# Kernel tuning notes

Measured on AMD Instinct MI355X. Metric: run time of the kernel, lower is better.

The kernel has to match this reference:

```python
import jax, jax.numpy as jnp
import numpy as np

N_NODES = 50000
N_EDGES = 800000
D_NODE = 64
D_EDGE = 64
D_OUT = 64
D_HID = 128
LN_EPS = 1e-5


def _mlp_params(key, d_in):
    # layer sizes: [d_in, D_HID, D_HID, D_OUT]; weights stored [in, out]
    ks = jax.random.split(key, 3)
    dims = [d_in, D_HID, D_HID, D_OUT]
    params = []
    for i in range(3):
        s = 1.0 / np.sqrt(dims[i])
        params.append(jax.random.uniform(ks[i], (dims[i], dims[i + 1]), minval=-s, maxval=s, dtype=jnp.float32))
        params.append(jnp.zeros((dims[i + 1],), jnp.float32))
    # LayerNorm gamma/beta
    params.append(jnp.ones((D_OUT,), jnp.float32))
    params.append(jnp.zeros((D_OUT,), jnp.float32))
    return params


def _mlp_ln(h, W0, b0, W1, b1, W2, b2, g, beta):
    h = jax.nn.relu(h @ W0 + b0)
    h = jax.nn.relu(h @ W1 + b1)
    h = h @ W2 + b2
    mu = jnp.mean(h, axis=-1, keepdims=True)
    var = jnp.mean(jnp.square(h - mu), axis=-1, keepdims=True)
    return (h - mu) * jax.lax.rsqrt(var + LN_EPS) * g + beta


def setup_inputs() -> dict:
    key = jax.random.key(0)
    k = jax.random.split(key, 8)
    inp = {
        "x": jax.random.normal(k[0], (N_NODES, D_NODE), jnp.float32),
        "mesh_edge_index": jax.random.randint(k[1], (2, N_EDGES), 0, N_NODES, dtype=jnp.int32),
        "mesh_edge_attr": jax.random.normal(k[2], (N_EDGES, D_EDGE), jnp.float32),
        "world_edge_index": jax.random.randint(k[3], (2, N_EDGES), 0, N_NODES, dtype=jnp.int32),
        "world_edge_attr": jax.random.normal(k[4], (N_EDGES, D_EDGE), jnp.float32),
    }
    names = ["W0", "b0", "W1", "b1", "W2", "b2", "ln_g", "ln_b"]
    for pref, kk, d_in in [("mesh", k[5], 2 * D_NODE + D_EDGE),
                           ("world", k[6], 2 * D_NODE + D_EDGE),
                           ("upd", k[7], D_NODE + 2 * D_OUT)]:
        ps = _mlp_params(kk, d_in)
        for nm, p in zip(names, ps):
            inp[f"{pref}_{nm}"] = p
    return inp


def _edge_block(x, edge_index, edge_attr, W0, b0, W1, b1, W2, b2, g, beta):
    src, dst = edge_index[0], edge_index[1]  # PyG: x_j = source, x_i = target
    x_i = x[dst]  # [E, D_NODE]
    x_j = x[src]
    concat = jnp.concatenate([x_i, x_j, edge_attr], axis=-1)  # [E, 2D+De]
    new_edge = edge_attr + _mlp_ln(concat, W0, b0, W1, b1, W2, b2, g, beta)
    agg = jax.ops.segment_sum(new_edge, dst, num_segments=N_NODES)  # 'add' aggr at target
    return agg, new_edge


def reference(x, mesh_edge_index, mesh_edge_attr, world_edge_index, world_edge_attr,
              mesh_W0, mesh_b0, mesh_W1, mesh_b1, mesh_W2, mesh_b2, mesh_ln_g, mesh_ln_b,
              world_W0, world_b0, world_W1, world_b1, world_W2, world_b2, world_ln_g, world_ln_b,
              upd_W0, upd_b0, upd_W1, upd_b1, upd_W2, upd_b2, upd_ln_g, upd_ln_b):
    agg_m, new_edge_m = _edge_block(x, mesh_edge_index, mesh_edge_attr,
                                    mesh_W0, mesh_b0, mesh_W1, mesh_b1, mesh_W2, mesh_b2, mesh_ln_g, mesh_ln_b)
    agg_w, new_edge_w = _edge_block(x, world_edge_index, world_edge_attr,
                                    world_W0, world_b0, world_W1, world_b1, world_W2, world_b2, world_ln_g, world_ln_b)
    concat = jnp.concatenate([x, agg_m, agg_w], axis=-1)  # [N, D_NODE + 2*D_OUT]
    x_new = x + _mlp_ln(concat, upd_W0, upd_b0, upd_W1, upd_b1, upd_W2, upd_b2, upd_ln_g, upd_ln_b)
    return x_new, new_edge_m, new_edge_w
```

## Files before the change

kernel.cpp:

```cpp
#include <hip/hip_runtime.h>


#define NNODES 50000
#define NEDGES 800000
#define NBLK 512

typedef __bf16 bf16x8 __attribute__((ext_vector_type(8)));
typedef float f32x4 __attribute__((ext_vector_type(4)));
#define MFMA(a, b, c) __builtin_amdgcn_mfma_f32_16x16x32_bf16(a, b, c, 0, 0, 0)

#define OFF_A 0
#define OFF_H0 24576
#define OFF_O OFF_H0
#define OFF_SA 40960
#define OFF_P 57600
#define OFF_IX 59648
#define OFF_PAR 59904
#define SMEM 61696

__device__ __forceinline__ unsigned short f2bf(float f) {
  unsigned u = __builtin_bit_cast(unsigned, f);
  u = (u + 0x7fffu + ((u >> 16) & 1u)) >> 16;
  return (unsigned short)u;
}
__device__ __forceinline__ float bf2f(unsigned short h) {
  return __builtin_bit_cast(float, (unsigned)h << 16);
}
__device__ __forceinline__ unsigned long long pk4(f32x4 v) {
  union { unsigned short h[4]; unsigned long long u; } p;
  p.h[0] = f2bf(v[0]); p.h[1] = f2bf(v[1]); p.h[2] = f2bf(v[2]); p.h[3] = f2bf(v[3]);
  return p.u;
}
__device__ __forceinline__ void cvt8s(float4 f0, float4 f1, char* d) {
  union { unsigned short us[8]; int4 v; } u;
  u.us[0] = f2bf(f0.x); u.us[1] = f2bf(f0.y); u.us[2] = f2bf(f0.z); u.us[3] = f2bf(f0.w);
  u.us[4] = f2bf(f1.x); u.us[5] = f2bf(f1.y); u.us[6] = f2bf(f1.z); u.us[7] = f2bf(f1.w);
  *(int4*)d = u.v;
}

template <bool EDGE>
__global__ __launch_bounds__(512, 4) void mlp_block(
    const float* __restrict__ g1, const float* __restrict__ g2,
    const float* __restrict__ g3, const int* __restrict__ srcI,
    const int* __restrict__ dstI, const unsigned short* __restrict__ Wt,
    const float* __restrict__ b0, const float* __restrict__ b1,
    const float* __restrict__ b2, const float* __restrict__ gam,
    const float* __restrict__ bet, float* __restrict__ outp,
    float* __restrict__ agg, int M) {
  __shared__ __align__(16) char sm[SMEM];
  const int tid = threadIdx.x, lane = tid & 63, wave = tid >> 6;
  const int lrow = lane & 15, cg = lane >> 4;
  const unsigned short* Wt0 = Wt;
  const unsigned short* Wt1 = Wt + 24576;
  const unsigned short* Wt2 = Wt + 40960;
  const int ntiles = (M + 63) >> 6;

  const int cg2 = wave & 3, rg = wave >> 2;

  for (int i = tid; i < 448; i += 512) {
    float v;
    if (i < 128) v = b0[i];
    else if (i < 256) v = b1[i - 128];
    else if (i < 320) v = b2[i - 256];
    else if (i < 384) v = gam[i - 320];
    else v = bet[i - 384];
    ((float*)(sm + OFF_PAR))[i] = v;
  }
  const float* PAR = (const float*)(sm + OFF_PAR);

  bf16x8 w0f[6], w1f[4], w2f[4];
#pragma unroll
  for (int kk = 0; kk < 6; ++kk)
    w0f[kk] = *(const bf16x8*)(Wt0 + (wave * 16 + lrow) * 192 + kk * 32 + cg * 8);
#pragma unroll
  for (int kk = 0; kk < 4; ++kk)
    w1f[kk] = *(const bf16x8*)(Wt1 + (wave * 16 + lrow) * 128 + kk * 32 + cg * 8);
#pragma unroll
  for (int kk = 0; kk < 4; ++kk)
    w2f[kk] = *(const bf16x8*)(Wt2 + (cg2 * 16 + lrow) * 128 + kk * 32 + cg * 8);

  const int srow = (tid >> 5) * 4 + ((tid & 31) >> 3), oct = tid & 7;

  int t = blockIdx.x;
  if (t >= ntiles) return;

  float4 ga0, ga1, gb0, gb1;
  int dcur = 0;
  {
    int row = t * 64 + srow;
    int r1, r2;
    if (EDGE) { dcur = dstI[row]; r1 = dcur; r2 = srcI[row]; }
    else { int rr = min(row, M - 1); r1 = rr; r2 = rr; }
    const float* p1 = g1 + (size_t)r1 * 64 + oct * 8;
    const float* p2 = g2 + (size_t)r2 * 64 + oct * 8;
    ga0 = *(const float4*)p1; ga1 = *(const float4*)(p1 + 4);
    gb0 = *(const float4*)p2; gb1 = *(const float4*)(p2 + 4);
#pragma unroll
    for (int i = 0; i < 2; ++i) {
      int chunk = wave * 2 + i;
      const float* gsrc;
      if (EDGE) gsrc = g3 + (size_t)t * 4096 + chunk * 256 + lane * 4;
      else { int gr = min(t * 64 + chunk * 4 + (lane >> 4), M - 1); gsrc = g3 + (size_t)gr * 64 + (lane & 15) * 4; }
      __builtin_amdgcn_global_load_lds((const __attribute__((address_space(1))) unsigned int*)gsrc,
          (__attribute__((address_space(3))) unsigned int*)(sm + OFF_SA + chunk * 1040), 16, 0, 0);
    }
  }

  for (; t < ntiles; t += NBLK) {
    const int tn = t + NBLK;
    const bool more = tn < ntiles;
    __syncthreads();
    {
      char* a0 = sm + OFF_A + srow * 384;
      const int swz = (srow & 7) << 4;
      cvt8s(ga0, ga1, a0 + ((oct * 16) ^ swz));
      cvt8s(gb0, gb1, a0 + ((128 + oct * 16) ^ swz));
      const char* sa = sm + OFF_SA + (srow >> 2) * 1040 + (srow & 3) * 256 + oct * 32;
      float4 c0 = *(const float4*)sa, c1 = *(const float4*)(sa + 16);
      cvt8s(c0, c1, a0 + ((256 + oct * 16) ^ swz));
      if (EDGE && (tid & 7) == 0) ((int*)(sm + OFF_IX))[srow] = dcur;
    }
    int dn = 0, sn = 0;
    if (EDGE && more) { int row = tn * 64 + srow; dn = dstI[row]; sn = srcI[row]; }
    __syncthreads();
    if (more) {
      const float *p1, *p2;
      if (EDGE) {
        p1 = g1 + (size_t)dn * 64 + oct * 8;
        p2 = g2 + (size_t)sn * 64 + oct * 8;
        dcur = dn;
      } else {
        int rr = min(tn * 64 + srow, M - 1);
        p1 = g1 + (size_t)rr * 64 + oct * 8;
        p2 = g2 + (size_t)rr * 64 + oct * 8;
      }
      ga0 = *(const float4*)p1; ga1 = *(const float4*)(p1 + 4);
      gb0 = *(const float4*)p2; gb1 = *(const float4*)(p2 + 4);
#pragma unroll
      for (int i = 0; i < 2; ++i) {
        int chunk = wave * 2 + i;
        const float* gsrc;
        if (EDGE) gsrc = g3 + (size_t)tn * 4096 + chunk * 256 + lane * 4;
        else { int gr = min(tn * 64 + chunk * 4 + (lane >> 4), M - 1); gsrc = g3 + (size_t)gr * 64 + (lane & 15) * 4; }
        __builtin_amdgcn_global_load_lds((const __attribute__((address_space(1))) unsigned int*)gsrc,
            (__attribute__((address_space(3))) unsigned int*)(sm + OFF_SA + chunk * 1040), 16, 0, 0);
      }
    }
    {
      const f32x4 bb0 = *(const f32x4*)(PAR + wave * 16 + cg * 4);
#pragma unroll
      for (int rt = 0; rt < 4; ++rt) {
        const int row = rt * 16 + lrow, swz = (row & 7) << 4;
        const char* ab = sm + OFF_A + row * 384;
        f32x4 acc = {0.f, 0.f, 0.f, 0.f};
#pragma unroll
        for (int kk = 0; kk < 6; ++kk)
          acc = MFMA(w0f[kk], *(const bf16x8*)(ab + ((kk * 64 + cg * 16) ^ swz)), acc);
        f32x4 h;
#pragma unroll
        for (int q = 0; q < 4; ++q) h[q] = fmaxf(acc[q] + bb0[q], 0.f);
        *(unsigned long long*)(sm + OFF_H0 + row * 256 + ((wave * 32 + cg * 8) ^ swz)) = pk4(h);
      }
    }
    __syncthreads();
    {
      const f32x4 bb1 = *(const f32x4*)(PAR + 128 + wave * 16 + cg * 4);
#pragma unroll
      for (int rt = 0; rt < 4; ++rt) {
        const int row = rt * 16 + lrow, swz = (row & 7) << 4;
        const char* hb = sm + OFF_H0 + row * 256;
        f32x4 acc = {0.f, 0.f, 0.f, 0.f};
#pragma unroll
        for (int kk = 0; kk < 4; ++kk)
          acc = MFMA(w1f[kk], *(const bf16x8*)(hb + ((kk * 64 + cg * 16) ^ swz)), acc);
        f32x4 h;
#pragma unroll
        for (int q = 0; q < 4; ++q) h[q] = fmaxf(acc[q] + bb1[q], 0.f);
        *(unsigned long long*)(sm + OFF_A + row * 384 + ((wave * 32 + cg * 8) ^ swz)) = pk4(h);
      }
    }
    __syncthreads();
    f32x4 accE[2];
    {
      const f32x4 bb2 = *(const f32x4*)(PAR + 256 + cg2 * 16 + cg * 4);
#pragma unroll
      for (int j = 0; j < 2; ++j) {
        const int rt = rg * 2 + j, row = rt * 16 + lrow, swz = (row & 7) << 4;
        const char* hb = sm + OFF_A + row * 384;
        f32x4 acc = {0.f, 0.f, 0.f, 0.f};
#pragma unroll
        for (int kk = 0; kk < 4; ++kk)
          acc = MFMA(w2f[kk], *(const bf16x8*)(hb + ((kk * 64 + cg * 16) ^ swz)), acc);
#pragma unroll
        for (int q = 0; q < 4; ++q) acc[q] += bb2[q];
        float s = acc[0] + acc[1] + acc[2] + acc[3];
        float ss = acc[0] * acc[0] + acc[1] * acc[1] + acc[2] * acc[2] + acc[3] * acc[3];
        s += __shfl_xor(s, 16, 64); s += __shfl_xor(s, 32, 64);
        ss += __shfl_xor(ss, 16, 64); ss += __shfl_xor(ss, 32, 64);
        if (cg == 0) *(float2*)(sm + OFF_P + row * 32 + cg2 * 8) = make_float2(s, ss);
        accE[j] = acc;
      }
    }
    __syncthreads();
    {
      const f32x4 gv = *(const f32x4*)(PAR + 320 + cg2 * 16 + cg * 4);
      const f32x4 bv = *(const f32x4*)(PAR + 384 + cg2 * 16 + cg * 4);
#pragma unroll
      for (int j = 0; j < 2; ++j) {
        const int rt = rg * 2 + j, row = rt * 16 + lrow;
        float4 p0 = *(const float4*)(sm + OFF_P + row * 32);
        float4 p1 = *(const float4*)(sm + OFF_P + row * 32 + 16);
        float s = p0.x + p0.z + p1.x + p1.z, ss = p0.y + p0.w + p1.y + p1.w;
        float mean = s * (1.f / 64.f);
        float var = fmaxf(ss * (1.f / 64.f) - mean * mean, 0.f);
        float inv = rsqrtf(var + 1e-5f);
        const int swz = (row & 7) << 4;
        unsigned long long rv =
            *(const unsigned long long*)(sm + OFF_A + row * 384 + ((256 + cg2 * 32 + cg * 8) ^ swz));
        f32x4 a = accE[j];
        f32x4 o;
        o[0] = (a[0] - mean) * inv * gv[0] + bv[0] + bf2f((unsigned short)rv);
        o[1] = (a[1] - mean) * inv * gv[1] + bv[1] + bf2f((unsigned short)(rv >> 16));
        o[2] = (a[2] - mean) * inv * gv[2] + bv[2] + bf2f((unsigned short)(rv >> 32));
        o[3] = (a[3] - mean) * inv * gv[3] + bv[3] + bf2f((unsigned short)(rv >> 48));
        *(f32x4*)(sm + OFF_O + row * 256 + ((cg2 * 64 + cg * 16) ^ ((row & 15) << 4))) = o;
      }
    }
    __syncthreads();
#pragma unroll
    for (int j = 0; j < 2; ++j) {
      const int row = wave * 8 + j * 4 + cg, gr = t * 64 + row;
      const int cq = lrow;
      const bool ok = EDGE || gr < M;
      f32x4 v = *(const f32x4*)(sm + OFF_O + row * 256 + ((cq * 16) ^ ((row & 15) << 4)));
      if (ok) *(f32x4*)(outp + (size_t)gr * 64 + cq * 4) = v;
      if (EDGE) {
        const int d = ((const int*)(sm + OFF_IX))[row];
        float* ap = agg + (size_t)d * 64;
#pragma unroll
        for (int k = 0; k < 4; ++k) {
          float sv = *(const float*)(sm + OFF_O + row * 256 + (((cq + k * 16) * 4) ^ ((row & 15) << 4)));
          atomicAdd(ap + cq + k * 16, sv);
        }
      }
    }
  }
}

struct PrepArgs { const float* w[9]; unsigned short* wt[3]; };

__global__ void prep_w(PrepArgs pa) {
  int i = blockIdx.x * 256 + threadIdx.x;
  if (i >= 3 * 49152) return;
  int mlp = i / 49152;
  int rem = i - mlp * 49152;
  int mat, off, K, N;
  if (rem < 24576)      { mat = 0; off = 0;     K = 192; N = 128; }
  else if (rem < 40960) { mat = 1; off = 24576; K = 128; N = 128; }
  else                  { mat = 2; off = 40960; K = 128; N = 64;  }
  int local = rem - off;
  int n = local / K, k = local - n * K;
  if (mlp == 2 && mat == 0) k = (k + 64) % 192;
  pa.wt[mlp][rem] = f2bf(pa.w[mlp * 3 + mat][k * N + n]);
}

__global__ void zero_f4(float4* p, int n) {
  int i = blockIdx.x * blockDim.x + threadIdx.x;
  if (i < n) p[i] = make_float4(0.f, 0.f, 0.f, 0.f);
}

extern "C" void kernel_launch(void* const* d_in, const int* in_sizes, int n_in,
                              void* d_out, int out_size, void* d_ws, size_t ws_size,
                              hipStream_t stream) {
  const float* x      = (const float*)d_in[0];
  const int*   meIdx  = (const int*)d_in[1];
  const float* meAttr = (const float*)d_in[2];
  const int*   weIdx  = (const int*)d_in[3];
  const float* weAttr = (const float*)d_in[4];

  float* out_x  = (float*)d_out;
  float* out_em = out_x + (size_t)NNODES * 64;
  float* out_ew = out_em + (size_t)NEDGES * 64;

  char* ws = (char*)d_ws;
  unsigned short* WtM = (unsigned short*)ws;
  unsigned short* WtW = (unsigned short*)(ws + 98304);
  unsigned short* WtU = (unsigned short*)(ws + 196608);
  float* aggm = (float*)(ws + 294912);
  float* aggw = aggm + (size_t)NNODES * 64;

  zero_f4<<<dim3(6250), dim3(256), 0, stream>>>((float4*)aggm, 1600000);

  PrepArgs pa;
  for (int m = 0; m < 3; ++m)
    for (int l = 0; l < 3; ++l)
      pa.w[m * 3 + l] = (const float*)d_in[5 + m * 8 + l * 2];
  pa.wt[0] = WtM; pa.wt[1] = WtW; pa.wt[2] = WtU;
  prep_w<<<dim3(576), dim3(256), 0, stream>>>(pa);

  mlp_block<true><<<dim3(NBLK), dim3(512), 0, stream>>>(
      x, x, meAttr, meIdx, meIdx + NEDGES, WtM,
      (const float*)d_in[6], (const float*)d_in[8], (const float*)d_in[10],
      (const float*)d_in[11], (const float*)d_in[12],
      out_em, aggm, NEDGES);
  mlp_block<true><<<dim3(NBLK), dim3(512), 0, stream>>>(
      x, x, weAttr, weIdx, weIdx + NEDGES, WtW,
      (const float*)d_in[14], (const float*)d_in[16], (const float*)d_in[18],
      (const float*)d_in[19], (const float*)d_in[20],
      out_ew, aggw, NEDGES);
  mlp_block<false><<<dim3(NBLK), dim3(512), 0, stream>>>(
      aggm, aggw, x, nullptr, nullptr, WtU,
      (const float*)d_in[22], (const float*)d_in[24], (const float*)d_in[26],
      (const float*)d_in[27], (const float*)d_in[28],
      out_x, nullptr, NNODES);
}
```

Before: 890.2 us.

## Counting-sort edges by destination and pre-reduce segments before atomic scatter

Adds histogram, scan and scatter kernels that build a destination-sorted permutation of edges for each edge set. The edge MLP kernels then read edges through this permutation and write outputs back to their original positions. Consecutive rows with the same destination inside a tile are summed in shared memory, so only one atomicAdd per run is issued instead of one per edge. This is meant to cut the global atomic traffic of the segment sum. In exchange it adds three preprocessing kernels, including a weakly parallel two-block scan, and turns the edge-attribute loads and output stores into indirect accesses.

```diff
diff --git a/kernel.cpp b/kernel.cpp
--- a/kernel.cpp
+++ b/kernel.cpp
@@ -42,7 +42,8 @@
 __global__ __launch_bounds__(512, 4) void mlp_block(
     const float* __restrict__ g1, const float* __restrict__ g2,
     const float* __restrict__ g3, const int* __restrict__ srcI,
-    const int* __restrict__ dstI, const unsigned short* __restrict__ Wt,
+    const int* __restrict__ perm, const int* __restrict__ dstS,
+    const unsigned short* __restrict__ Wt,
     const float* __restrict__ b0, const float* __restrict__ b1,
     const float* __restrict__ b2, const float* __restrict__ gam,
     const float* __restrict__ bet, float* __restrict__ outp,
@@ -89,8 +90,11 @@
   {
     int row = t * 64 + srow;
     int r1, r2;
-    if (EDGE) { dcur = dstI[row]; r1 = dcur; r2 = srcI[row]; }
-    else { int rr = min(row, M - 1); r1 = rr; r2 = rr; }
+    if (EDGE) {
+      int e = perm[row];
+      dcur = dstS[row];
+      r1 = dcur; r2 = srcI[e];
+    } else { int rr = min(row, M - 1); r1 = rr; r2 = rr; }
     const float* p1 = g1 + (size_t)r1 * 64 + oct * 8;
     const float* p2 = g2 + (size_t)r2 * 64 + oct * 8;
     ga0 = *(const float4*)p1; ga1 = *(const float4*)(p1 + 4);
@@ -99,8 +103,10 @@
     for (int i = 0; i < 2; ++i) {
       int chunk = wave * 2 + i;
       const float* gsrc;
-      if (EDGE) gsrc = g3 + (size_t)t * 4096 + chunk * 256 + lane * 4;
-      else { int gr = min(t * 64 + chunk * 4 + (lane >> 4), M - 1); gsrc = g3 + (size_t)gr * 64 + (lane & 15) * 4; }
+      if (EDGE) {
+        int er = perm[t * 64 + chunk * 4 + (lane >> 4)];
+        gsrc = g3 + (size_t)er * 64 + (lane & 15) * 4;
+      } else { int gr = min(t * 64 + chunk * 4 + (lane >> 4), M - 1); gsrc = g3 + (size_t)gr * 64 + (lane & 15) * 4; }
       __builtin_amdgcn_global_load_lds((const __attribute__((address_space(1))) unsigned int*)gsrc,
           (__attribute__((address_space(3))) unsigned int*)(sm + OFF_SA + chunk * 1040), 16, 0, 0);
     }
@@ -121,7 +127,11 @@
       if (EDGE && (tid & 7) == 0) ((int*)(sm + OFF_IX))[srow] = dcur;
     }
     int dn = 0, sn = 0;
-    if (EDGE && more) { int row = tn * 64 + srow; dn = dstI[row]; sn = srcI[row]; }
+    if (EDGE && more) {
+      int row = tn * 64 + srow;
+      int e = perm[row];
+      dn = dstS[row]; sn = srcI[e];
+    }
     __syncthreads();
     if (more) {
       const float *p1, *p2;
@@ -140,8 +150,10 @@
       for (int i = 0; i < 2; ++i) {
         int chunk = wave * 2 + i;
         const float* gsrc;
-        if (EDGE) gsrc = g3 + (size_t)tn * 4096 + chunk * 256 + lane * 4;
-        else { int gr = min(tn * 64 + chunk * 4 + (lane >> 4), M - 1); gsrc = g3 + (size_t)gr * 64 + (lane & 15) * 4; }
+        if (EDGE) {
+          int er = perm[tn * 64 + chunk * 4 + (lane >> 4)];
+          gsrc = g3 + (size_t)er * 64 + (lane & 15) * 4;
+        } else { int gr = min(tn * 64 + chunk * 4 + (lane >> 4), M - 1); gsrc = g3 + (size_t)gr * 64 + (lane & 15) * 4; }
         __builtin_amdgcn_global_load_lds((const __attribute__((address_space(1))) unsigned int*)gsrc,
             (__attribute__((address_space(3))) unsigned int*)(sm + OFF_SA + chunk * 1040), 16, 0, 0);
       }
@@ -231,17 +243,39 @@
     for (int j = 0; j < 2; ++j) {
       const int row = wave * 8 + j * 4 + cg, gr = t * 64 + row;
       const int cq = lrow;
-      const bool ok = EDGE || gr < M;
       f32x4 v = *(const f32x4*)(sm + OFF_O + row * 256 + ((cq * 16) ^ ((row & 15) << 4)));
-      if (ok) *(f32x4*)(outp + (size_t)gr * 64 + cq * 4) = v;
       if (EDGE) {
-        const int d = ((const int*)(sm + OFF_IX))[row];
-        float* ap = agg + (size_t)d * 64;
-#pragma unroll
-        for (int k = 0; k < 4; ++k) {
-          float sv = *(const float*)(sm + OFF_O + row * 256 + (((cq + k * 16) * 4) ^ ((row & 15) << 4)));
-          atomicAdd(ap + cq + k * 16, sv);
+        const int e = perm[gr];
+        *(f32x4*)(outp + (size_t)e * 64 + cq * 4) = v;
+        const int* ix = (const int*)(sm + OFF_IX);
+        const int d = ix[row];
+        const bool head = (row == 0) || (ix[row - 1] != d);
+        if (head) {
+          float a0, a1, a2, a3;
+          {
+            const int swz = (row & 15) << 4;
+            a0 = *(const float*)(sm + OFF_O + row * 256 + ((cq * 4) ^ swz));
+            a1 = *(const float*)(sm + OFF_O + row * 256 + (((cq + 16) * 4) ^ swz));
+            a2 = *(const float*)(sm + OFF_O + row * 256 + (((cq + 32) * 4) ^ swz));
+            a3 = *(const float*)(sm + OFF_O + row * 256 + (((cq + 48) * 4) ^ swz));
+          }
+          int r2 = row + 1;
+          while (r2 < 64 && ix[r2] == d) {
+            const int swz = (r2 & 15) << 4;
+            a0 += *(const float*)(sm + OFF_O + r2 * 256 + ((cq * 4) ^ swz));
+            a1 += *(const float*)(sm + OFF_O + r2 * 256 + (((cq + 16) * 4) ^ swz));
+            a2 += *(const float*)(sm + OFF_O + r2 * 256 + (((cq + 32) * 4) ^ swz));
+            a3 += *(const float*)(sm + OFF_O + r2 * 256 + (((cq + 48) * 4) ^ swz));
+            ++r2;
+          }
+          float* ap = agg + (size_t)d * 64;
+          atomicAdd(ap + cq, a0);
+          atomicAdd(ap + cq + 16, a1);
+          atomicAdd(ap + cq + 32, a2);
+          atomicAdd(ap + cq + 48, a3);
         }
+      } else {
+        if (gr < M) *(f32x4*)(outp + (size_t)gr * 64 + cq * 4) = v;
       }
     }
   }
@@ -269,6 +303,50 @@
   if (i < n) p[i] = make_float4(0.f, 0.f, 0.f, 0.f);
 }
 
+__global__ void hist_k(const int* __restrict__ dM, const int* __restrict__ dW,
+                       int* __restrict__ curM, int* __restrict__ curW, int E) {
+  int i = blockIdx.x * 256 + threadIdx.x;
+  if (i < E) {
+    atomicAdd(curM + dM[i], 1);
+    atomicAdd(curW + dW[i], 1);
+  }
+}
+
+__global__ __launch_bounds__(1024) void scan_k(int* __restrict__ curM, int* __restrict__ curW) {
+  __shared__ int buf[1024];
+  int* cur = blockIdx.x ? curW : curM;
+  const int tid = threadIdx.x, base = tid * 49;
+  const int lim = min(base + 49, NNODES);
+  int p = 0;
+  for (int b = base; b < lim; ++b) p += cur[b];
+  buf[tid] = p;
+  __syncthreads();
+  const int own = p;
+  for (int off = 1; off < 1024; off <<= 1) {
+    int nv = (tid >= off) ? buf[tid - off] : 0;
+    __syncthreads();
+    buf[tid] += nv;
+    __syncthreads();
+  }
+  int running = buf[tid] - own;
+  for (int b = base; b < lim; ++b) { int h = cur[b]; cur[b] = running; running += h; }
+}
+
+__global__ void scatter_k(const int* __restrict__ dM, const int* __restrict__ dW,
+                          int* __restrict__ curM, int* __restrict__ curW,
+                          int* __restrict__ permM, int* __restrict__ dstSM,
+                          int* __restrict__ permW, int* __restrict__ dstSW, int E) {
+  int i = blockIdx.x * 256 + threadIdx.x;
+  if (i < E) {
+    int d = dM[i];
+    int p = atomicAdd(curM + d, 1);
+    permM[p] = i; dstSM[p] = d;
+    d = dW[i];
+    p = atomicAdd(curW + d, 1);
+    permW[p] = i; dstSW[p] = d;
+  }
+}
+
 extern "C" void kernel_launch(void* const* d_in, const int* in_sizes, int n_in,
                               void* d_out, int out_size, void* d_ws, size_t ws_size,
                               hipStream_t stream) {
@@ -288,8 +366,15 @@
   unsigned short* WtU = (unsigned short*)(ws + 196608);
   float* aggm = (float*)(ws + 294912);
   float* aggw = aggm + (size_t)NNODES * 64;
+  int* curM  = (int*)(ws + 294912 + 25600000);
+  int* curW  = curM + NNODES;
+  int* permM = (int*)(ws + 294912 + 25600000 + 400000);
+  int* dstSM = permM + NEDGES;
+  int* permW = dstSM + NEDGES;
+  int* dstSW = permW + NEDGES;
 
   zero_f4<<<dim3(6250), dim3(256), 0, stream>>>((float4*)aggm, 1600000);
+  zero_f4<<<dim3(98), dim3(256), 0, stream>>>((float4*)curM, 25000);
 
   PrepArgs pa;
   for (int m = 0; m < 3; ++m)
@@ -298,18 +383,23 @@
   pa.wt[0] = WtM; pa.wt[1] = WtW; pa.wt[2] = WtU;
   prep_w<<<dim3(576), dim3(256), 0, stream>>>(pa);
 
+  hist_k<<<dim3(3125), dim3(256), 0, stream>>>(meIdx + NEDGES, weIdx + NEDGES, curM, curW, NEDGES);
+  scan_k<<<dim3(2), dim3(1024), 0, stream>>>(curM, curW);
+  scatter_k<<<dim3(3125), dim3(256), 0, stream>>>(meIdx + NEDGES, weIdx + NEDGES, curM, curW,
+                                                  permM, dstSM, permW, dstSW, NEDGES);
+
   mlp_block<true><<<dim3(NBLK), dim3(512), 0, stream>>>(
-      x, x, meAttr, meIdx, meIdx + NEDGES, WtM,
+      x, x, meAttr, meIdx, permM, dstSM, WtM,
       (const float*)d_in[6], (const float*)d_in[8], (const float*)d_in[10],
       (const float*)d_in[11], (const float*)d_in[12],
       out_em, aggm, NEDGES);
   mlp_block<true><<<dim3(NBLK), dim3(512), 0, stream>>>(
-      x, x, weAttr, weIdx, weIdx + NEDGES, WtW,
+      x, x, weAttr, weIdx, permW, dstSW, WtW,
       (const float*)d_in[14], (const float*)d_in[16], (const float*)d_in[18],
       (const float*)d_in[19], (const float*)d_in[20],
       out_ew, aggw, NEDGES);
   mlp_block<false><<<dim3(NBLK), dim3(512), 0, stream>>>(
-      aggm, aggw, x, nullptr, nullptr, WtU,
+      aggm, aggw, x, nullptr, nullptr, nullptr, WtU,
       (const float*)d_in[22], (const float*)d_in[24], (const float*)d_in[26],
       (const float*)d_in[27], (const float*)d_in[28],
       out_x, nullptr, NNODES);
```

Measured after the change: 1.270 ms. 42.7% more time.
